# Optimization experiments

Hardware: AMD Instinct MI355X
Metric: run time of the kernel (lower is better)

## Reference

```python
import jax, jax.numpy as jnp
import numpy as np

B = 4096   # batch
I = 1024   # in_features
O = 1024   # out_features
N = 4      # LUT fan-in; table size 2**N = 16


def setup_inputs() -> dict:
    key = jax.random.key(0)
    k1, k2, k3 = jax.random.split(key, 3)
    return {
        "x": jax.random.normal(k1, (B, I), dtype=jnp.float32),
        # learnable mapping logits: (out_features, n, in_features)
        "mapping_logits": jax.random.normal(k2, (O, N, I), dtype=jnp.float32),
        # per-node LUT tables with 2**n corner values each
        "lut_tables": jax.random.normal(k3, (O, 2 ** N), dtype=jnp.float32),
    }


def reference(x, mapping_logits, lut_tables):
    # softmax-weighted input selection: (B,I) x (O,N,I) -> (B,O,N)
    w = jax.nn.softmax(mapping_logits, axis=-1)
    selected = jnp.einsum('bi,oni->bon', x, w)
    # BatchedLUTNodes: squash to [0,1], multilinear interpolation over 2**N corners
    s = jax.nn.sigmoid(selected)                      # (B,O,N)
    cw = jnp.ones(s.shape[:2] + (1,), dtype=s.dtype)  # corner weights, grows to (B,O,2**N)
    for j in range(N):                                # fixed small loop over fan-in
        sj = s[..., j][..., None]                     # (B,O,1)
        cw = jnp.concatenate([cw * (1.0 - sj), cw * sj], axis=-1)
    # weighted sum of per-node table entries -> (B,O)
    return jnp.einsum('boc,oc->bo', cw, lut_tables)
```

## Files before the change

kernel.cpp:

```cpp
#include <hip/hip_runtime.h>

#define B_DIM 4096
#define I_DIM 1024
#define O_DIM 1024
#define ON_DIM 4096
#define TILE_HALFS 4096

typedef _Float16 half8   __attribute__((ext_vector_type(8)));
typedef float    floatx16 __attribute__((ext_vector_type(16)));

__global__ __launch_bounds__(256)
void ltn_prep1(const float* __restrict__ logits, const float* __restrict__ x,
               float2* __restrict__ stats, _Float16* __restrict__ xt) {
  const int t = threadIdx.x;
  if (blockIdx.x < 1024) {
    const int lane = t & 63, wv = t >> 6;
    const int row = blockIdx.x * 4 + wv;
    const float4* src = (const float4*)(logits + (size_t)row * I_DIM);
    float4 v[4];
#pragma unroll
    for (int j = 0; j < 4; j++) v[j] = src[j * 64 + lane];
    float m = -1e30f;
#pragma unroll
    for (int j = 0; j < 4; j++)
      m = fmaxf(m, fmaxf(fmaxf(v[j].x, v[j].y), fmaxf(v[j].z, v[j].w)));
#pragma unroll
    for (int off = 1; off < 64; off <<= 1) m = fmaxf(m, __shfl_xor(m, off));
    float s = 0.0f;
#pragma unroll
    for (int j = 0; j < 4; j++) {
      s += __expf(v[j].x - m) + __expf(v[j].y - m)
         + __expf(v[j].z - m) + __expf(v[j].w - m);
    }
#pragma unroll
    for (int off = 1; off < 64; off <<= 1) s += __shfl_xor(s, off);
    if (lane == 0) stats[row] = make_float2(m, 1.0f / s);
  } else {
    const int bid = blockIdx.x - 1024;
    const int mb = bid >> 5, kt = bid & 31;
    const int nn = t >> 1, hf = t & 1;
    const int row = mb * 128 + nn;
    const float4* src = (const float4*)(x + (size_t)row * I_DIM + kt * 32 + hf * 16);
    const float4 a = src[0], b = src[1], c = src[2], d = src[3];
    half8 h0, h1;
    h0[0] = (_Float16)a.x; h0[1] = (_Float16)a.y; h0[2] = (_Float16)a.z; h0[3] = (_Float16)a.w;
    h0[4] = (_Float16)b.x; h0[5] = (_Float16)b.y; h0[6] = (_Float16)b.z; h0[7] = (_Float16)b.w;
    h1[0] = (_Float16)c.x; h1[1] = (_Float16)c.y; h1[2] = (_Float16)c.z; h1[3] = (_Float16)c.w;
    h1[4] = (_Float16)d.x; h1[5] = (_Float16)d.y; h1[6] = (_Float16)d.z; h1[7] = (_Float16)d.w;
    _Float16* base = xt + ((size_t)mb * 32 + kt) * TILE_HALFS + (hf * 2) * 1024 + nn * 8;
    *(half8*)base = h0;
    *(half8*)(base + 1024) = h1;
  }
}

__global__ __launch_bounds__(256)
void ltn_prep2(const float* __restrict__ logits, const float2* __restrict__ stats,
               _Float16* __restrict__ wt) {
  const int t  = threadIdx.x;
  const int nn = t >> 1, hf = t & 1;
  const int nb = blockIdx.x >> 5, kb = blockIdx.x & 31;
  const int row = nb * 128 + nn;
  const float2 st = stats[row];
  const float4* src = (const float4*)(logits + (size_t)row * I_DIM + kb * 32 + hf * 16);
  const float4 a = src[0], b = src[1], c = src[2], d = src[3];
  half8 h0, h1;
  h0[0] = (_Float16)(__expf(a.x - st.x) * st.y);
  h0[1] = (_Float16)(__expf(a.y - st.x) * st.y);
  h0[2] = (_Float16)(__expf(a.z - st.x) * st.y);
  h0[3] = (_Float16)(__expf(a.w - st.x) * st.y);
  h0[4] = (_Float16)(__expf(b.x - st.x) * st.y);
  h0[5] = (_Float16)(__expf(b.y - st.x) * st.y);
  h0[6] = (_Float16)(__expf(b.z - st.x) * st.y);
  h0[7] = (_Float16)(__expf(b.w - st.x) * st.y);
  h1[0] = (_Float16)(__expf(c.x - st.x) * st.y);
  h1[1] = (_Float16)(__expf(c.y - st.x) * st.y);
  h1[2] = (_Float16)(__expf(c.z - st.x) * st.y);
  h1[3] = (_Float16)(__expf(c.w - st.x) * st.y);
  h1[4] = (_Float16)(__expf(d.x - st.x) * st.y);
  h1[5] = (_Float16)(__expf(d.y - st.x) * st.y);
  h1[6] = (_Float16)(__expf(d.z - st.x) * st.y);
  h1[7] = (_Float16)(__expf(d.w - st.x) * st.y);
  _Float16* base = wt + ((size_t)nb * 32 + kb) * TILE_HALFS + (hf * 2) * 1024 + nn * 8;
  *(half8*)base = h0;
  *(half8*)(base + 1024) = h1;
}

__global__ __launch_bounds__(256, 4)
void ltn_gemm_lut(const _Float16* __restrict__ xt,
                  const _Float16* __restrict__ wt,
                  const float* __restrict__ lut,
                  float* __restrict__ out) {
  __shared__ _Float16 As[2][4][128][8];

  const int tid  = threadIdx.x;
  const int lane = tid & 63;
  const int wv   = tid >> 6;
  const int wr   = wv >> 1;
  const int wc   = wv & 1;
  const int mb   = blockIdx.x;
  const int nb   = blockIdx.y;
  const int l31  = lane & 31;
  const int lhi  = lane >> 5;

  const _Float16* baseA = xt + (size_t)mb * 32 * TILE_HALFS;
  const _Float16* pB = wt + (size_t)nb * 32 * TILE_HALFS
                     + lhi * 1024 + (wc * 64 + l31) * 8;

  floatx16 acc[2][2];
#pragma unroll
  for (int i = 0; i < 2; i++)
#pragma unroll
    for (int j = 0; j < 2; j++) acc[i][j] = (floatx16)0.0f;

  auto stageA = [&](int buf, int kt) {
#pragma unroll
    for (int s = 0; s < 2; s++) {
      const int c = wv * 2 + s;
      const _Float16* g = baseA + (size_t)kt * TILE_HALFS + c * 512 + lane * 8;
      __builtin_amdgcn_global_load_lds(
          (const __attribute__((address_space(1))) void*)g,
          (__attribute__((address_space(3))) void*)((char*)&As[buf][0][0][0] + c * 1024),
          16, 0, 0);
    }
  };
  auto loadB = [&](int kt, half8* bf) {
    const half8* p = (const half8*)(pB + (size_t)kt * TILE_HALFS);
    bf[0] = p[0];
    bf[1] = p[32];
    bf[2] = p[256];
    bf[3] = p[288];
  };

  half8 bfc[4], bfn[4];
  stageA(0, 0);
  loadB(0, bfc);
  int buf = 0;
  for (int kt = 0; kt < 32; kt++) {
    __syncthreads();
    if (kt + 1 < 32) { stageA(buf ^ 1, kt + 1); loadB(kt + 1, bfn); }
#pragma unroll
    for (int s = 0; s < 2; s++) {
      const int kb = s * 2 + lhi;
      half8 af[2];
#pragma unroll
      for (int tm = 0; tm < 2; tm++) {
        const int rr = wr * 2 + tm;
        af[tm] = *(const half8*)&As[buf][kb][rr * 32 + l31][0];
      }
#pragma unroll
      for (int tm = 0; tm < 2; tm++)
#pragma unroll
        for (int tn = 0; tn < 2; tn++)
          acc[tm][tn] = __builtin_amdgcn_mfma_f32_32x32x16_f16(
              af[tm], bfc[s * 2 + tn], acc[tm][tn], 0, 0, 0);
    }
#pragma unroll
    for (int q = 0; q < 4; q++) bfc[q] = bfn[q];
    buf ^= 1;
  }

#pragma unroll
  for (int tn = 0; tn < 2; tn++) {
    const int o = (nb * 128 + wc * 64 + tn * 32 + l31) >> 2;
    const float4* lt4 = (const float4*)(lut + (size_t)o * 16);
    const float4 L0 = lt4[0], L1 = lt4[1], L2 = lt4[2], L3 = lt4[3];
#pragma unroll
    for (int tm = 0; tm < 2; tm++) {
#pragma unroll
      for (int r = 0; r < 16; r++) {
        const float v  = acc[tm][tn][r];
        const float sv = 1.0f / (1.0f + __expf(-v));
        const float s1 = __shfl_down(sv, 1);
        const float s2 = __shfl_down(sv, 2);
        const float s3 = __shfl_down(sv, 3);
        if ((lane & 3) == 0) {
          const float s0 = sv;
          const float a0 = L0.x + (L2.x - L0.x) * s3;
          const float a1 = L0.y + (L2.y - L0.y) * s3;
          const float a2 = L0.z + (L2.z - L0.z) * s3;
          const float a3 = L0.w + (L2.w - L0.w) * s3;
          const float a4 = L1.x + (L3.x - L1.x) * s3;
          const float a5 = L1.y + (L3.y - L1.y) * s3;
          const float a6 = L1.z + (L3.z - L1.z) * s3;
          const float a7 = L1.w + (L3.w - L1.w) * s3;
          const float b0 = a0 + (a4 - a0) * s2;
          const float b1 = a1 + (a5 - a1) * s2;
          const float b2 = a2 + (a6 - a2) * s2;
          const float b3 = a3 + (a7 - a3) * s2;
          const float c0 = b0 + (b2 - b0) * s1;
          const float c1 = b1 + (b3 - b1) * s1;
          const float res = c0 + (c1 - c0) * s0;
          const int row = mb * 128 + wr * 64 + tm * 32
                        + (r & 3) + 8 * (r >> 2) + 4 * lhi;
          out[(size_t)row * O_DIM + o] = res;
        }
      }
    }
  }
}

extern "C" void kernel_launch(void* const* d_in, const int* in_sizes, int n_in,
                              void* d_out, int out_size, void* d_ws, size_t ws_size,
                              hipStream_t stream) {
  const float* x      = (const float*)d_in[0];
  const float* logits = (const float*)d_in[1];
  const float* lut    = (const float*)d_in[2];
  float* out          = (float*)d_out;

  _Float16* wt = (_Float16*)d_ws;
  _Float16* xt = (_Float16*)d_ws + (size_t)ON_DIM * I_DIM;
  float2* stats = (float2*)d_out;

  ltn_prep1<<<2048, 256, 0, stream>>>(logits, x, stats, xt);
  ltn_prep2<<<1024, 256, 0, stream>>>(logits, stats, wt);
  dim3 grid(32, 32);
  ltn_gemm_lut<<<grid, 256, 0, stream>>>(xt, wt, lut, out);
}
```

Baseline: 140.3 us.

## Restage prep kernels through LDS with 16-row slabs and adjust GEMM tiled layout

The prep kernels now read full contiguous 1024-wide rows (16 rows per block), convert to fp16, transpose through padded shared memory, and write 16x1024 slabs in a new tiled layout. The GEMM's A staging and B fragment addressing are rewritten to match the new slab layout. The aim is to coalesce global reads and writes in the prep stage and launch fewer, larger blocks. In exchange the prep kernels take on an LDS round-trip and a barrier, and prep1 now allocates shared memory even for its softmax-stats blocks.

```diff
diff --git a/kernel.cpp b/kernel.cpp
--- a/kernel.cpp
+++ b/kernel.cpp
@@ -4,14 +4,17 @@
 #define I_DIM 1024
 #define O_DIM 1024
 #define ON_DIM 4096
-#define TILE_HALFS 4096
 
 typedef _Float16 half8   __attribute__((ext_vector_type(8)));
+typedef _Float16 half4_t __attribute__((ext_vector_type(4)));
 typedef float    floatx16 __attribute__((ext_vector_type(16)));
+
+#define SLAB 136
 
 __global__ __launch_bounds__(256)
 void ltn_prep1(const float* __restrict__ logits, const float* __restrict__ x,
                float2* __restrict__ stats, _Float16* __restrict__ xt) {
+  __shared__ _Float16 lds[128 * SLAB];
   const int t = threadIdx.x;
   if (blockIdx.x < 1024) {
     const int lane = t & 63, wv = t >> 6;
@@ -36,53 +39,54 @@
     for (int off = 1; off < 64; off <<= 1) s += __shfl_xor(s, off);
     if (lane == 0) stats[row] = make_float2(m, 1.0f / s);
   } else {
-    const int bid = blockIdx.x - 1024;
-    const int mb = bid >> 5, kt = bid & 31;
-    const int nn = t >> 1, hf = t & 1;
-    const int row = mb * 128 + nn;
-    const float4* src = (const float4*)(x + (size_t)row * I_DIM + kt * 32 + hf * 16);
-    const float4 a = src[0], b = src[1], c = src[2], d = src[3];
-    half8 h0, h1;
-    h0[0] = (_Float16)a.x; h0[1] = (_Float16)a.y; h0[2] = (_Float16)a.z; h0[3] = (_Float16)a.w;
-    h0[4] = (_Float16)b.x; h0[5] = (_Float16)b.y; h0[6] = (_Float16)b.z; h0[7] = (_Float16)b.w;
-    h1[0] = (_Float16)c.x; h1[1] = (_Float16)c.y; h1[2] = (_Float16)c.z; h1[3] = (_Float16)c.w;
-    h1[4] = (_Float16)d.x; h1[5] = (_Float16)d.y; h1[6] = (_Float16)d.z; h1[7] = (_Float16)d.w;
-    _Float16* base = xt + ((size_t)mb * 32 + kt) * TILE_HALFS + (hf * 2) * 1024 + nn * 8;
-    *(half8*)base = h0;
-    *(half8*)(base + 1024) = h1;
+    const int g    = blockIdx.x - 1024;
+    const int slab = t >> 1;
+    const int jo   = (t & 1) * 4;
+#pragma unroll
+    for (int i = 0; i < 16; i++) {
+      const float4 v = *(const float4*)(x + (size_t)(g * 16 + i) * I_DIM + t * 4);
+      half4_t h;
+      h[0] = (_Float16)v.x; h[1] = (_Float16)v.y;
+      h[2] = (_Float16)v.z; h[3] = (_Float16)v.w;
+      *(half4_t*)&lds[slab * SLAB + i * 8 + jo] = h;
+    }
+    __syncthreads();
+    _Float16* dst = xt + (size_t)g * 16384;
+#pragma unroll
+    for (int s = 0; s < 8; s++) {
+      const int h = s * 2048 + t * 8;
+      *(half8*)(dst + h) = *(const half8*)&lds[(h >> 7) * SLAB + (h & 127)];
+    }
   }
 }
 
 __global__ __launch_bounds__(256)
 void ltn_prep2(const float* __restrict__ logits, const float2* __restrict__ stats,
                _Float16* __restrict__ wt) {
-  const int t  = threadIdx.x;
-  const int nn = t >> 1, hf = t & 1;
-  const int nb = blockIdx.x >> 5, kb = blockIdx.x & 31;
-  const int row = nb * 128 + nn;
-  const float2 st = stats[row];
-  const float4* src = (const float4*)(logits + (size_t)row * I_DIM + kb * 32 + hf * 16);
-  const float4 a = src[0], b = src[1], c = src[2], d = src[3];
-  half8 h0, h1;
-  h0[0] = (_Float16)(__expf(a.x - st.x) * st.y);
-  h0[1] = (_Float16)(__expf(a.y - st.x) * st.y);
-  h0[2] = (_Float16)(__expf(a.z - st.x) * st.y);
-  h0[3] = (_Float16)(__expf(a.w - st.x) * st.y);
-  h0[4] = (_Float16)(__expf(b.x - st.x) * st.y);
-  h0[5] = (_Float16)(__expf(b.y - st.x) * st.y);
-  h0[6] = (_Float16)(__expf(b.z - st.x) * st.y);
-  h0[7] = (_Float16)(__expf(b.w - st.x) * st.y);
-  h1[0] = (_Float16)(__expf(c.x - st.x) * st.y);
-  h1[1] = (_Float16)(__expf(c.y - st.x) * st.y);
-  h1[2] = (_Float16)(__expf(c.z - st.x) * st.y);
-  h1[3] = (_Float16)(__expf(c.w - st.x) * st.y);
-  h1[4] = (_Float16)(__expf(d.x - st.x) * st.y);
-  h1[5] = (_Float16)(__expf(d.y - st.x) * st.y);
-  h1[6] = (_Float16)(__expf(d.z - st.x) * st.y);
-  h1[7] = (_Float16)(__expf(d.w - st.x) * st.y);
-  _Float16* base = wt + ((size_t)nb * 32 + kb) * TILE_HALFS + (hf * 2) * 1024 + nn * 8;
-  *(half8*)base = h0;
-  *(half8*)(base + 1024) = h1;
+  __shared__ _Float16 lds[128 * SLAB];
+  const int t    = threadIdx.x;
+  const int g    = blockIdx.x;
+  const int slab = t >> 1;
+  const int jo   = (t & 1) * 4;
+#pragma unroll
+  for (int i = 0; i < 16; i++) {
+    const int row = g * 16 + i;
+    const float2 st = stats[row];
+    const float4 v = *(const float4*)(logits + (size_t)row * I_DIM + t * 4);
+    half4_t h;
+    h[0] = (_Float16)(__expf(v.x - st.x) * st.y);
+    h[1] = (_Float16)(__expf(v.y - st.x) * st.y);
+    h[2] = (_Float16)(__expf(v.z - st.x) * st.y);
+    h[3] = (_Float16)(__expf(v.w - st.x) * st.y);
+    *(half4_t*)&lds[slab * SLAB + i * 8 + jo] = h;
+  }
+  __syncthreads();
+  _Float16* dst = wt + (size_t)g * 16384;
+#pragma unroll
+  for (int s = 0; s < 8; s++) {
+    const int h = s * 2048 + t * 8;
+    *(half8*)(dst + h) = *(const half8*)&lds[(h >> 7) * SLAB + (h & 127)];
+  }
 }
 
 __global__ __launch_bounds__(256, 4)
@@ -90,7 +94,7 @@
                   const _Float16* __restrict__ wt,
                   const float* __restrict__ lut,
                   float* __restrict__ out) {
-  __shared__ _Float16 As[2][4][128][8];
+  __shared__ _Float16 As[2][8][512];
 
   const int tid  = threadIdx.x;
   const int lane = tid & 63;
@@ -102,9 +106,9 @@
   const int l31  = lane & 31;
   const int lhi  = lane >> 5;
 
-  const _Float16* baseA = xt + (size_t)mb * 32 * TILE_HALFS;
-  const _Float16* pB = wt + (size_t)nb * 32 * TILE_HALFS
-                     + lhi * 1024 + (wc * 64 + l31) * 8;
+  const _Float16* pB = wt
+      + ((size_t)(nb * 8 + wc * 4 + (l31 >> 4)) * 32) * 512
+      + lhi * 128 + (l31 & 15) * 8;
 
   floatx16 acc[2][2];
 #pragma unroll
@@ -116,19 +120,18 @@
 #pragma unroll
     for (int s = 0; s < 2; s++) {
       const int c = wv * 2 + s;
-      const _Float16* g = baseA + (size_t)kt * TILE_HALFS + c * 512 + lane * 8;
+      const _Float16* g = xt + ((size_t)((mb * 8 + c) * 32 + kt)) * 512 + lane * 8;
       __builtin_amdgcn_global_load_lds(
           (const __attribute__((address_space(1))) void*)g,
-          (__attribute__((address_space(3))) void*)((char*)&As[buf][0][0][0] + c * 1024),
-          16, 0, 0);
+          (__attribute__((address_space(3))) void*)&As[buf][c][0], 16, 0, 0);
     }
   };
   auto loadB = [&](int kt, half8* bf) {
-    const half8* p = (const half8*)(pB + (size_t)kt * TILE_HALFS);
+    const half8* p = (const half8*)(pB + (size_t)kt * 512);
     bf[0] = p[0];
-    bf[1] = p[32];
-    bf[2] = p[256];
-    bf[3] = p[288];
+    bf[1] = p[4096];
+    bf[2] = p[32];
+    bf[3] = p[4128];
   };
 
   half8 bfc[4], bfn[4];
@@ -144,8 +147,8 @@
       half8 af[2];
 #pragma unroll
       for (int tm = 0; tm < 2; tm++) {
-        const int rr = wr * 2 + tm;
-        af[tm] = *(const half8*)&As[buf][kb][rr * 32 + l31][0];
+        const int cb = wr * 4 + tm * 2 + (l31 >> 4);
+        af[tm] = *(const half8*)&As[buf][cb][kb * 128 + (l31 & 15) * 8];
       }
 #pragma unroll
       for (int tm = 0; tm < 2; tm++)
@@ -211,8 +214,8 @@
   _Float16* xt = (_Float16*)d_ws + (size_t)ON_DIM * I_DIM;
   float2* stats = (float2*)d_out;
 
-  ltn_prep1<<<2048, 256, 0, stream>>>(logits, x, stats, xt);
-  ltn_prep2<<<1024, 256, 0, stream>>>(logits, stats, wt);
+  ltn_prep1<<<1280, 256, 0, stream>>>(logits, x, stats, xt);
+  ltn_prep2<<<256, 256, 0, stream>>>(logits, stats, wt);
   dim3 grid(32, 32);
   ltn_gemm_lut<<<grid, 256, 0, stream>>>(xt, wt, lut, out);
 }
```

After: 136.9 us. -2.5%, faster.
